# Optimization experiments

Measured on AMD Instinct MI355X. Metric: run time of the kernel, lower is better.

The kernel has to match this reference:

```python
import math
import jax, jax.numpy as jnp
import numpy as np

D_MODEL = 2048
D_INNER = 4096   # expand * d_model
D_STATE = 16
D_CONV = 4
DT_RANK = 128    # d_model / 16
SCALE_X = 0.05         # conv1d input (int8) scale
SCALE_CONV_OUT = 0.05  # conv1d output (int8) scale


def quant(x, scale):
    """Simulated int8 quantize -> dequantize (as in the W4A8 pipeline)."""
    return jnp.clip(jnp.round(x / scale), -128.0, 127.0) * scale


def fwht(x):
    """Normalized fast Walsh-Hadamard transform over the last axis (power of 2)."""
    d = x.shape[-1]
    shp = x.shape
    x = x.reshape(-1, d)
    h = 1
    while h < d:
        x = x.reshape(-1, d // (2 * h), 2, h)
        a, s = x[:, :, 0, :], x[:, :, 1, :]
        x = jnp.stack([a + s, a - s], axis=2).reshape(-1, d)
        h *= 2
    return (x * (d ** -0.5)).reshape(shp)


def setup_inputs() -> dict:
    key = jax.random.key(0)
    ks = jax.random.split(key, 10)
    b, l = 2, 1024
    dt0 = jnp.exp(jax.random.uniform(ks[6], (D_INNER,), minval=math.log(1e-3), maxval=math.log(1e-1)))
    dt_bias = dt0 + jnp.log(-jnp.expm1(-dt0))  # inverse softplus of dt0
    A = -jnp.tile(jnp.arange(1.0, D_STATE + 1.0, dtype=jnp.float32), (D_INNER, 1))
    return {
        "hidden_states": jax.random.normal(ks[0], (b, l, D_MODEL), jnp.float32),
        "W_in": (jax.random.normal(ks[1], (2 * D_INNER, D_MODEL), jnp.float32) * 0.02),
        "conv_w": (jax.random.normal(ks[2], (D_INNER, D_CONV), jnp.float32) * 0.2),
        "conv_b": (jax.random.normal(ks[3], (D_INNER,), jnp.float32) * 0.02),
        "W_x": (jax.random.normal(ks[4], (DT_RANK + 2 * D_STATE, D_INNER), jnp.float32) * 0.02),
        "W_dt": (jax.random.normal(ks[5], (D_INNER, DT_RANK), jnp.float32) * 0.02),
        "dt_bias": dt_bias.astype(jnp.float32),
        "A": A.astype(jnp.float32),
        "D": jnp.ones((D_INNER,), jnp.float32),
        "W_out": (jax.random.normal(ks[7], (D_MODEL, D_INNER), jnp.float32) * 0.02),
    }


def reference(hidden_states, W_in, conv_w, conv_b, W_x, W_dt, dt_bias, A, D, W_out):
    b, l, dm = hidden_states.shape
    # in_proj -> seqlen-last layout, chunk into x (conv path) and z (gate)
    xz = jnp.einsum('bld,ed->bel', hidden_states, W_in)  # [b, 2*d_inner, l]
    x, z = jnp.split(xz, 2, axis=1)                      # [b, d_inner, l] each
    x = quant(x, SCALE_X)                                # int8 activation sim
    # fused causal depthwise conv1d + SiLU + requantize (quant_causal_conv1d)
    xp = jnp.pad(x, ((0, 0), (0, 0), (D_CONV - 1, 0)))
    xc = jax.lax.conv_general_dilated(
        xp, conv_w[:, None, :], (1,), 'VALID',
        dimension_numbers=('NCH', 'OIH', 'NCH'), feature_group_count=D_INNER)
    u = quant(jax.nn.silu(xc + conv_b[None, :, None]), SCALE_CONV_OUT)  # [b,d,l]
    # x_proj -> dt, B, C
    x_dbl = jnp.einsum('bdl,ed->ble', u, W_x)            # [b, l, dt_rank+2n]
    dt_in, B, C = jnp.split(x_dbl, [DT_RANK, DT_RANK + D_STATE], axis=-1)
    dt = jax.nn.softplus(jnp.einsum('blr,dr->bld', dt_in, W_dt) + dt_bias)  # [b,l,d]
    # selective scan: h_t = exp(dt*A) h_{t-1} + dt*B*u ; y = C.h + D*u
    xs = (dt.transpose(1, 0, 2),          # [l,b,d]
          u.transpose(2, 0, 1),           # [l,b,d]
          B.transpose(1, 0, 2),           # [l,b,n]
          C.transpose(1, 0, 2))           # [l,b,n]
    h0 = jnp.zeros((b, D_INNER, D_STATE), hidden_states.dtype)

    def step(h, inp):
        dt_t, u_t, B_t, C_t = inp
        dA = jnp.exp(dt_t[..., None] * A)                       # [b,d,n]
        h = dA * h + (dt_t * u_t)[..., None] * B_t[:, None, :]  # [b,d,n]
        return h, jnp.einsum('bdn,bn->bd', h, C_t)

    _, ys = jax.lax.scan(step, h0, xs)                    # ys: [l,b,d]
    y = ys.transpose(1, 2, 0) + D[:, None] * u            # [b,d,l]
    y = y * jax.nn.silu(z)                                # gated output
    y = fwht(y.transpose(0, 2, 1))                        # Hadamard over channels
    return jnp.einsum('ble,de->bld', y, W_out)            # out_proj -> [b,l,d_model]
```

## Files before the change

### kernel.cpp

```cpp
#include <hip/hip_runtime.h>
#include <math.h>

#define BB 2
#define LL 1024
#define DMODEL 2048
#define DI 4096
#define NSTATE 16
#define RANK 128
#define MM (BB*LL)
#define XE (2*DI)
#define EDBL (RANK + 2*NSTATE)
#define NWORDS (MM*DI/32)
#define NC 16
#define CL (LL/NC)

typedef __bf16 bf16x8 __attribute__((ext_vector_type(8)));
typedef __bf16 bf16x4 __attribute__((ext_vector_type(4)));
typedef float  f32x4  __attribute__((ext_vector_type(4)));

__device__ __forceinline__ float quant005(float x) {
    float q = rintf(x / 0.05f);
    q = fminf(fmaxf(q, -128.f), 127.f);
    return q * 0.05f;
}
__device__ __forceinline__ float softplusf(float x) {
    return fmaxf(x, 0.f) + log1pf(expf(-fabsf(x)));
}

__global__ __launch_bounds__(256) void reduce4g_kernel(
    const float* __restrict__ p, const float* __restrict__ Xx, float* __restrict__ out)
{
    const int gid = blockIdx.x * 256 + threadIdx.x;
    const int m = gid >> 11, c = gid & (DMODEL - 1);
    out[gid] = p[gid] + p[gid + (size_t)MM * DMODEL]
             + Xx[(size_t)m * XE + c] + Xx[(size_t)m * XE + DMODEL + c];
}

__global__ __launch_bounds__(256) void reduce6_kernel(
    const float* __restrict__ p, float* __restrict__ xdbl,
    __bf16* __restrict__ XdH, __bf16* __restrict__ XdM)
{
    const int gid = blockIdx.x * 256 + threadIdx.x;
    const size_t S = (size_t)MM * EDBL;
    float v = p[gid];
    #pragma unroll
    for (int s = 1; s < 6; ++s) v += p[gid + s * S];
    xdbl[gid] = v;
    const int m = gid / EDBL, e = gid - m * EDBL;
    if (e < RANK) {
        const __bf16 h = (__bf16)v;
        XdH[(size_t)m * RANK + e] = h;
        XdM[(size_t)m * RANK + e] = (__bf16)(v - (float)h);
    }
}

__global__ __launch_bounds__(256) void conv_kernel(
    const float* __restrict__ X, const float* __restrict__ conv_w,
    const float* __restrict__ conv_b, float* __restrict__ u,
    __bf16* __restrict__ uh, __bf16* __restrict__ um)
{
    const int gid = blockIdx.x * 256 + threadIdx.x;
    const int bl = gid >> 12, d = gid & (DI - 1);
    const int l = bl & (LL - 1);
    const float4 w4 = *(const float4*)(conv_w + 4 * d);
    const float wk[4] = {w4.x, w4.y, w4.z, w4.w};
    float acc = 0.f;
    #pragma unroll
    for (int k = 0; k < 4; ++k) {
        const int lp = l - 3 + k;
        if (lp >= 0) acc = fmaf(X[(size_t)(bl - 3 + k) * XE + d], wk[k], acc);
    }
    const float v = acc + conv_b[d];
    const float s = v / (1.f + expf(-v));
    const float q = quant005(s);
    u[gid] = q;
    const __bf16 h = (__bf16)q;
    uh[gid] = h;
    um[gid] = (__bf16)(q - (float)h);
}

__global__ __launch_bounds__(256) void scan_p1(
    const float* __restrict__ dtb, const float* __restrict__ u,
    const float* __restrict__ xdbl,
    float* __restrict__ hend, float* __restrict__ S)
{
    const int bx = blockIdx.x;
    const int c  = bx & (NC - 1);
    const int dg = (bx >> 4) & 255;
    const int b  = bx >> 12;
    const int dl = threadIdx.x >> 4, n = threadIdx.x & 15;
    const int d  = (dg << 4) + dl;
    const int t0 = c * CL;
    const float* dtp = dtb + ((size_t)b * LL + t0) * DI + d;
    const float* up  = u   + ((size_t)b * LL + t0) * DI + d;
    const float* xe  = xdbl + ((size_t)b * LL + t0) * EDBL;
    const float An = -(float)(n + 1);
    float h = 0.f, s = 0.f;
    for (int t = 0; t < CL; ++t) {
        const float dt = dtp[(size_t)t * DI];
        const float uv = up[(size_t)t * DI];
        const float Bn = xe[t * EDBL + RANK + n];
        const float w = __expf(dt * An);
        h = fmaf(h, w, dt * uv * Bn);
        s += dt;
    }
    hend[(((size_t)b * DI + d) * NC + c) * 16 + n] = h;
    if (n == 0) S[((size_t)b * DI + d) * NC + c] = s;
}

__global__ __launch_bounds__(256) void scan_p2(
    float* __restrict__ hend, const float* __restrict__ S)
{
    const int gid = blockIdx.x * 256 + threadIdx.x;
    const int n  = gid & 15;
    const int bd = gid >> 4;
    const float An = -(float)(n + 1);
    float* hp = hend + (size_t)bd * NC * 16 + n;
    const float* Sp = S + (size_t)bd * NC;
    float h = 0.f;
    for (int c = 0; c < NC; ++c) {
        const float he = hp[c * 16];
        const float P  = __expf(An * Sp[c]);
        hp[c * 16] = h;
        h = fmaf(h, P, he);
    }
}

__global__ __launch_bounds__(256) void scan_p3(
    const float* __restrict__ dtb, const float* __restrict__ u,
    const float* __restrict__ xdbl, const float* __restrict__ Dvec,
    const float* __restrict__ hin, float* __restrict__ X)
{
    const int bx = blockIdx.x;
    const int c  = bx & (NC - 1);
    const int dg = (bx >> 4) & 255;
    const int b  = bx >> 12;
    const int dl = threadIdx.x >> 4, n = threadIdx.x & 15;
    const int d  = (dg << 4) + dl;
    const int t0 = c * CL;
    const float* dtp = dtb + ((size_t)b * LL + t0) * DI + d;
    const float* up  = u   + ((size_t)b * LL + t0) * DI + d;
    const float* xe  = xdbl + ((size_t)b * LL + t0) * EDBL;
    float* Xp = X + ((size_t)b * LL + t0) * XE + d;
    const float Dv = Dvec[d];
    const float An = -(float)(n + 1);
    float h = hin[(((size_t)b * DI + d) * NC + c) * 16 + n];
    for (int t = 0; t < CL; ++t) {
        const float dt = dtp[(size_t)t * DI];
        const float uv = up[(size_t)t * DI];
        const float* e = xe + t * EDBL;
        const float Bn = e[RANK + n];
        const float Cn = e[RANK + NSTATE + n];
        const float w = __expf(dt * An);
        h = fmaf(h, w, dt * uv * Bn);
        float y = h * Cn;
        y += __shfl_xor(y, 1);
        y += __shfl_xor(y, 2);
        y += __shfl_xor(y, 4);
        y += __shfl_xor(y, 8);
        if (n == 0) {
            const float z = Xp[(size_t)t * XE + DI];
            const float sz = z / (1.f + __expf(-z));
            Xp[(size_t)t * XE] = (y + Dv * uv) * sz;
        }
    }
}

__device__ __forceinline__ void bfy8(float* a)
{
    float t;
    t = a[0]; a[0] = t + a[1]; a[1] = t - a[1];
    t = a[2]; a[2] = t + a[3]; a[3] = t - a[3];
    t = a[4]; a[4] = t + a[5]; a[5] = t - a[5];
    t = a[6]; a[6] = t + a[7]; a[7] = t - a[7];
    t = a[0]; a[0] = t + a[2]; a[2] = t - a[2];
    t = a[1]; a[1] = t + a[3]; a[3] = t - a[3];
    t = a[4]; a[4] = t + a[6]; a[6] = t - a[6];
    t = a[5]; a[5] = t + a[7]; a[7] = t - a[7];
    t = a[0]; a[0] = t + a[4]; a[4] = t - a[4];
    t = a[1]; a[1] = t + a[5]; a[5] = t - a[5];
    t = a[2]; a[2] = t + a[6]; a[6] = t - a[6];
    t = a[3]; a[3] = t + a[7]; a[7] = t - a[7];
}
#define FWIDX(a) ((a) + ((a) >> 5))

__global__ __launch_bounds__(512) void fwht8_kernel(float* __restrict__ X)
{
    __shared__ float s[DI + DI / 32];
    const int tid = threadIdx.x;
    float* base = X + (size_t)blockIdx.x * XE;
    {
        float a[8];
        const float4 v0 = *(const float4*)(base + tid * 8);
        const float4 v1 = *(const float4*)(base + tid * 8 + 4);
        a[0] = v0.x; a[1] = v0.y; a[2] = v0.z; a[3] = v0.w;
        a[4] = v1.x; a[5] = v1.y; a[6] = v1.z; a[7] = v1.w;
        bfy8(a);
        const int p = FWIDX(tid * 8);
        *(float4*)(s + p)     = make_float4(a[0], a[1], a[2], a[3]);
        *(float4*)(s + p + 4) = make_float4(a[4], a[5], a[6], a[7]);
    }
    __syncthreads();
    {
        const int b = (tid >> 3) * 64 + (tid & 7);
        float a[8];
        #pragma unroll
        for (int j = 0; j < 8; ++j) a[j] = s[FWIDX(b + j * 8)];
        bfy8(a);
        #pragma unroll
        for (int j = 0; j < 8; ++j) s[FWIDX(b + j * 8)] = a[j];
    }
    __syncthreads();
    {
        const int b = (tid >> 6) * 512 + (tid & 63);
        float a[8];
        #pragma unroll
        for (int j = 0; j < 8; ++j) a[j] = s[FWIDX(b + j * 64)];
        bfy8(a);
        #pragma unroll
        for (int j = 0; j < 8; ++j) s[FWIDX(b + j * 64)] = a[j];
    }
    __syncthreads();
    {
        const int b = tid;
        float a[8];
        #pragma unroll
        for (int j = 0; j < 8; ++j) a[j] = s[FWIDX(b + j * 512)];
        bfy8(a);
        #pragma unroll
        for (int j = 0; j < 8; ++j) s[FWIDX(b + j * 512)] = a[j];
    }
    __syncthreads();
    const float sc = 1.f / 64.f;
    __bf16* Xh = (__bf16*)(base + DI);
    __bf16* Xm = (__bf16*)(base + DI + 2048);
    for (int i = tid * 2; i < DI; i += 1024) {
        const float v0 = s[FWIDX(i)] * sc, v1 = s[FWIDX(i + 1)] * sc;
        const __bf16 h0 = (__bf16)v0, h1 = (__bf16)v1;
        __bf16 hh[2]  = {h0, h1};
        __bf16 mm2[2] = {(__bf16)(v0 - (float)h0), (__bf16)(v1 - (float)h1)};
        *(short2*)&Xh[i] = *(short2*)hh;
        *(short2*)&Xm[i] = *(short2*)mm2;
    }
}

__global__ __launch_bounds__(256) void splitw_kernel(
    const float* __restrict__ W, __bf16* __restrict__ H, __bf16* __restrict__ L)
{
    const int gid = blockIdx.x * 256 + threadIdx.x;
    const float4 a = *(const float4*)(W + (size_t)gid * 4);
    const float af[4] = {a.x, a.y, a.z, a.w};
    bf16x4 h, l;
    #pragma unroll
    for (int i = 0; i < 4; ++i) {
        const __bf16 hh = (__bf16)af[i];
        h[i] = hh;
        l[i] = (__bf16)(af[i] - (float)hh);
    }
    *(bf16x4*)&H[(size_t)gid * 4] = h;
    *(bf16x4*)&L[(size_t)gid * 4] = l;
}

__global__ __launch_bounds__(256) void splitwx_kernel(
    const float* __restrict__ W, __bf16* __restrict__ H, __bf16* __restrict__ L)
{
    const int gid = blockIdx.x * 256 + threadIdx.x;
    const int row = gid >> 10, c4 = (gid & 1023) << 2;
    float4 a = make_float4(0.f, 0.f, 0.f, 0.f);
    if (row < EDBL) a = *(const float4*)(W + (size_t)row * DI + c4);
    const float af[4] = {a.x, a.y, a.z, a.w};
    bf16x4 h, l;
    #pragma unroll
    for (int i = 0; i < 4; ++i) {
        const __bf16 hh = (__bf16)af[i];
        h[i] = hh;
        l[i] = (__bf16)(af[i] - (float)hh);
    }
    *(bf16x4*)&H[(size_t)(row * DI + c4)] = h;
    *(bf16x4*)&L[(size_t)(row * DI + c4)] = l;
}

__global__ __launch_bounds__(256) void zeromask_kernel(unsigned* __restrict__ mask)
{
    const int gid = blockIdx.x * 256 + threadIdx.x;
    mask[gid] = 0u;
}

__device__ __forceinline__ void stage_tile(const __bf16* __restrict__ g, int ld,
                                           __bf16* lds, int tid)
{
    const int r = tid >> 2;
    const int c = (tid & 3) << 3;
    #pragma unroll
    for (int i = 0; i < 2; ++i) {
        const __bf16* src = g + (size_t)(r + i * 64) * ld + c;
        __builtin_amdgcn_global_load_lds(
            (const __attribute__((address_space(1))) void*)src,
            (__attribute__((address_space(3))) void*)(lds + (r + i * 64) * 32 + c),
            16, 0, 0);
    }
}

template<int EPI>
__global__ __launch_bounds__(256) void gemm3k(
    const __bf16* __restrict__ Ah, const __bf16* __restrict__ Am, int lda,
    const __bf16* __restrict__ Bh, const __bf16* __restrict__ Bm, int ldb,
    float* __restrict__ C, int N, int ldc, int K, int Kz,
    const float* __restrict__ bias)
{
    if (EPI == 2) C += (size_t)blockIdx.z * MM * ldc;
    __shared__ __bf16 sA[128 * 32];
    __shared__ __bf16 sB[128 * 32];
    const int tid  = threadIdx.x;
    const int lane = tid & 63, w = tid >> 6;
    const int wr = w >> 1, wc = w & 1;
    const int bm = blockIdx.y << 7, bn = blockIdx.x << 7;
    const int lr = lane & 15;
    const int kg = (lane >> 4) << 3;
    const int kbeg = blockIdx.z * Kz;

    f32x4 acc[4][4] = {};
    for (int k0 = kbeg; k0 < kbeg + Kz; k0 += 32) {
        const __bf16* Ap; const __bf16* Bp; int kk;
        if (k0 < K)          { Ap = Ah; Bp = Bh; kk = k0; }
        else if (k0 < 2 * K) { Ap = Ah; Bp = Bm; kk = k0 - K; }
        else                 { Ap = Am; Bp = Bh; kk = k0 - 2 * K; }
        stage_tile(Ap + (size_t)bm * lda + kk, lda, sA, tid);
        stage_tile(Bp + (size_t)bn * ldb + kk, ldb, sB, tid);
        __syncthreads();
        bf16x8 a[4], b[4];
        #pragma unroll
        for (int f = 0; f < 4; ++f) {
            a[f] = *(const bf16x8*)&sA[(wr * 64 + f * 16 + lr) * 32 + kg];
            b[f] = *(const bf16x8*)&sB[(wc * 64 + f * 16 + lr) * 32 + kg];
        }
        #pragma unroll
        for (int i = 0; i < 4; ++i)
            #pragma unroll
            for (int j = 0; j < 4; ++j)
                acc[i][j] = __builtin_amdgcn_mfma_f32_16x16x32_bf16(a[i], b[j], acc[i][j], 0, 0, 0);
        __syncthreads();
    }
    #pragma unroll
    for (int i = 0; i < 4; ++i)
        #pragma unroll
        for (int j = 0; j < 4; ++j) {
            const int col  = bn + wc * 64 + j * 16 + (lane & 15);
            const int row0 = bm + wr * 64 + i * 16 + (lane >> 4) * 4;
            #pragma unroll
            for (int r = 0; r < 4; ++r) {
                float v = acc[i][j][r];
                if (EPI == 4) v = softplusf(v + bias[col]);
                if (EPI != 2 || col < N)
                    C[(size_t)(row0 + r) * ldc + col] = v;
            }
        }
}

__device__ __forceinline__ void plane_sel2(int kt, int ktps,
    const __bf16* A0h, const __bf16* A0m, const __bf16* B0h, const __bf16* B0m,
    const __bf16*& Ap, const __bf16*& Bp, int& kc)
{
    if (kt < ktps)          { Ap = A0h; Bp = B0h; kc = kt * 64; }
    else if (kt < 2 * ktps) { Ap = A0h; Bp = B0m; kc = (kt - ktps) * 64; }
    else                    { Ap = A0m; Bp = B0h; kc = (kt - 2 * ktps) * 64; }
}

__device__ __forceinline__ int swz_off(int row, int l16)
{
    const int off = row * 32 + l16 * 8;
    return off ^ (((off >> 6) & 3) << 3);
}

__device__ __forceinline__ void stage_h(
    const __bf16* __restrict__ baseP, const int* goff, int kcol,
    __bf16* ldsHalf, const int* ldso)
{
    #pragma unroll
    for (int i = 0; i < 2; ++i)
        __builtin_amdgcn_global_load_lds(
            (const __attribute__((address_space(1))) void*)(baseP + goff[i] + kcol),
            (__attribute__((address_space(3))) void*)(ldsHalf + ldso[i]),
            16, 0, 0);
}

#define G1BAR  asm volatile("s_barrier" ::: "memory")
#define G1LGKM asm volatile("s_waitcnt lgkmcnt(0)" ::: "memory")
#define G1MFMA(N0, N1)                                                            \
    __builtin_amdgcn_s_setprio(1);                                                \
    _Pragma("unroll")                                                             \
    for (int f = 0; f < 8; ++f) {                                                 \
        acc[f][N0] = __builtin_amdgcn_mfma_f32_16x16x32_bf16(a[f], b0, acc[f][N0], 0, 0, 0); \
        acc[f][N1] = __builtin_amdgcn_mfma_f32_16x16x32_bf16(a[f], b1, acc[f][N1], 0, 0, 0); \
    }                                                                             \
    __builtin_amdgcn_s_setprio(0)

template<int EPI>
__global__ __launch_bounds__(512, 2) void gemm_8p(
    const __bf16* __restrict__ Ah, const __bf16* __restrict__ Am, int lda,
    const __bf16* __restrict__ Bh, const __bf16* __restrict__ Bm, int ldb,
    float* __restrict__ C0, float* __restrict__ C1,
    int ktps, unsigned* __restrict__ mask)
{
    __shared__ __bf16 lds[2][2][2][8192];
    const int tid = threadIdx.x;
    const int lane = tid & 63, w = tid >> 6;
    const int wr = w >> 2, wc = w & 3;
    const int bm = blockIdx.y << 8, bn = blockIdx.x << 8;
    const int lr = lane & 15, l16 = lane >> 4;
    const int T = 3 * ktps;
    const int zoff = (EPI == 2) ? (int)blockIdx.z * 1024 : 0;

    const __bf16* A0h = Ah + (size_t)bm * lda;
    const __bf16* A0m = Am + (size_t)bm * lda;
    const __bf16* B0h = Bh + (size_t)bn * ldb;
    const __bf16* B0m = Bm + (size_t)bn * ldb;

    int ga[2], gb[2], lo[2];
    #pragma unroll
    for (int i = 0; i < 2; ++i) {
        const int t = i * 512 + tid;
        const int row = t >> 2;
        const int gr = (t & 3) ^ ((t >> 3) & 3);
        ga[i] = row * lda + gr * 8;
        gb[i] = row * ldb + gr * 8;
        lo[i] = t * 8;
    }
    int sa[8], sb[4];
    #pragma unroll
    for (int f = 0; f < 8; ++f) sa[f] = swz_off(wr * 128 + f * 16 + lr, l16);
    #pragma unroll
    for (int nf = 0; nf < 4; ++nf) sb[nf] = swz_off(wc * 64 + nf * 16 + lr, l16);

    {
        const __bf16 *Ap, *Bp; int kc;
        plane_sel2(0, ktps, A0h, A0m, B0h, B0m, Ap, Bp, kc);
        stage_h(Ap, ga, zoff + kc +  0, (__bf16*)&lds[0][0][0][0], lo);
        stage_h(Bp, gb, zoff + kc +  0, (__bf16*)&lds[0][1][0][0], lo);
        stage_h(Ap, ga, zoff + kc + 32, (__bf16*)&lds[0][0][1][0], lo);
        stage_h(Bp, gb, zoff + kc + 32, (__bf16*)&lds[0][1][1][0], lo);
        plane_sel2(1, ktps, A0h, A0m, B0h, B0m, Ap, Bp, kc);
        stage_h(Ap, ga, zoff + kc +  0, (__bf16*)&lds[1][0][0][0], lo);
        stage_h(Bp, gb, zoff + kc +  0, (__bf16*)&lds[1][1][0][0], lo);
        stage_h(Ap, ga, zoff + kc + 32, (__bf16*)&lds[1][0][1][0], lo);
    }
    asm volatile("s_waitcnt vmcnt(6)" ::: "memory");
    G1BAR;

    f32x4 acc[8][4] = {};
    for (int kt = 0; kt < T; ++kt) {
        const int c = kt & 1;
        const __bf16* lA = &lds[c][0][0][0];
        const __bf16* lB = &lds[c][1][0][0];
        const __bf16 *Ap2, *Bp2; int kc2;
        plane_sel2(kt + 2 < T ? kt + 2 : T - 1, ktps, A0h, A0m, B0h, B0m, Ap2, Bp2, kc2);
        bf16x8 a[8], b0, b1;

        #pragma unroll
        for (int f = 0; f < 8; ++f) a[f] = *(const bf16x8*)(lA + sa[f]);
        b0 = *(const bf16x8*)(lB + sb[0]);
        b1 = *(const bf16x8*)(lB + sb[1]);
        if (kt + 1 < T) {
            const __bf16 *Ap1, *Bp1; int kc1;
            plane_sel2(kt + 1, ktps, A0h, A0m, B0h, B0m, Ap1, Bp1, kc1);
            stage_h(Bp1, gb, zoff + kc1 + 32, (__bf16*)&lds[c ^ 1][1][1][0], lo);
        }
        G1BAR; G1LGKM;
        G1MFMA(0, 1);
        G1BAR;

        b0 = *(const bf16x8*)(lB + sb[2]);
        b1 = *(const bf16x8*)(lB + sb[3]);
        if (kt + 2 < T)
            stage_h(Ap2, ga, zoff + kc2, (__bf16*)&lds[c][0][0][0], lo);
        G1BAR; G1LGKM;
        G1MFMA(2, 3);
        G1BAR;

        #pragma unroll
        for (int f = 0; f < 8; ++f) a[f] = *(const bf16x8*)(lA + 8192 + sa[f]);
        b0 = *(const bf16x8*)(lB + 8192 + sb[0]);
        b1 = *(const bf16x8*)(lB + 8192 + sb[1]);
        if (kt + 2 < T)
            stage_h(Bp2, gb, zoff + kc2, (__bf16*)&lds[c][1][0][0], lo);
        G1BAR; G1LGKM;
        G1MFMA(0, 1);
        G1BAR;

        b0 = *(const bf16x8*)(lB + 8192 + sb[2]);
        b1 = *(const bf16x8*)(lB + 8192 + sb[3]);
        if (kt + 2 < T)
            stage_h(Ap2, ga, zoff + kc2 + 32, (__bf16*)&lds[c][0][1][0], lo);
        if (kt < T - 2) { asm volatile("s_waitcnt vmcnt(6)" ::: "memory"); }
        else            { asm volatile("s_waitcnt vmcnt(0)" ::: "memory"); }
        G1BAR; G1LGKM;
        G1MFMA(2, 3);
        G1BAR;
    }

    float* Cp; int ldc;
    if (EPI == 1) { Cp = C0; ldc = XE; }
    else {
        if (blockIdx.z < 2) { Cp = C0 + (size_t)blockIdx.z * MM * DMODEL; ldc = DMODEL; }
        else                { Cp = C1 + (size_t)(blockIdx.z - 2) * DMODEL; ldc = XE; }
    }
    #pragma unroll
    for (int f = 0; f < 8; ++f)
        #pragma unroll
        for (int nf = 0; nf < 4; ++nf) {
            const int col  = bn + wc * 64 + nf * 16 + lr;
            const int row0 = bm + wr * 128 + f * 16 + l16 * 4;
            #pragma unroll
            for (int r = 0; r < 4; ++r) {
                float v = acc[f][nf][r];
                const int row = row0 + r;
                if (EPI == 1 && col < DI) {
                    const float fq = v / 0.05f;
                    const float q = rintf(fq);
                    if (0.5f - fabsf(fq - q) < 1e-3f) {
                        const int e = row * DI + col;
                        atomicOr(&mask[e >> 5], 1u << (e & 31));
                    }
                    v = fminf(fmaxf(q, -128.f), 127.f) * 0.05f;
                }
                Cp[(size_t)row * ldc + col] = v;
            }
        }
}

__global__ __launch_bounds__(256) void fixup_kernel(
    const float* __restrict__ hidden, const float* __restrict__ W_in,
    const unsigned* __restrict__ mask, float* __restrict__ X)
{
    const int gwave = (blockIdx.x * 256 + threadIdx.x) >> 6;
    const int lane  = threadIdx.x & 63;
    const int nwaves = gridDim.x * 4;
    for (int base = gwave * 64; base < NWORDS; base += nwaves * 64) {
        const unsigned myw = mask[base + lane];
        unsigned long long bal = __ballot(myw != 0u);
        while (bal) {
            const int src = __ffsll((unsigned long long)bal) - 1;
            bal &= bal - 1;
            unsigned word = __shfl(myw, src);
            const int widx = base + src;
            while (word) {
                const int bit = __ffs(word) - 1;
                word &= word - 1;
                const int e = widx * 32 + bit;
                const int m = e >> 12, n = e & (DI - 1);
                const float* ap = hidden + (size_t)m * DMODEL;
                const float* bp = W_in   + (size_t)n * DMODEL;
                float s = 0.f;
                #pragma unroll
                for (int kk = 0; kk < 8; ++kk) {
                    const int k = kk * 256 + lane * 4;
                    const float4 a = *(const float4*)(ap + k);
                    const float4 b = *(const float4*)(bp + k);
                    s += a.x * b.x + a.y * b.y + a.z * b.z + a.w * b.w;
                }
                s += __shfl_xor(s, 1);  s += __shfl_xor(s, 2);  s += __shfl_xor(s, 4);
                s += __shfl_xor(s, 8);  s += __shfl_xor(s, 16); s += __shfl_xor(s, 32);
                if (lane == 0) X[(size_t)m * XE + n] = quant005(s);
            }
        }
    }
}

extern "C" void kernel_launch(void* const* d_in, const int* in_sizes, int n_in,
                              void* d_out, int out_size, void* d_ws, size_t ws_size,
                              hipStream_t stream)
{
    const float* hidden  = (const float*)d_in[0];
    const float* W_in    = (const float*)d_in[1];
    const float* conv_w  = (const float*)d_in[2];
    const float* conv_b  = (const float*)d_in[3];
    const float* W_x     = (const float*)d_in[4];
    const float* W_dt    = (const float*)d_in[5];
    const float* dt_bias = (const float*)d_in[6];
    const float* Dvec    = (const float*)d_in[8];
    const float* W_out   = (const float*)d_in[9];
    float* out = (float*)d_out;

    float* X    = (float*)d_ws;
    float* u    = X + (size_t)MM * XE;
    float* xdbl = u + (size_t)MM * DI;
    float* dtb  = xdbl + (size_t)MM * EDBL;
    __bf16* WinH  = (__bf16*)u;
    __bf16* WinM  = (__bf16*)dtb;
    unsigned* mask = (unsigned*)xdbl;
    __bf16* uh = (__bf16*)dtb;
    __bf16* um = uh + (size_t)MM * DI;
    __bf16* WoutH = (__bf16*)dtb;
    __bf16* WoutM = WoutH + (size_t)DMODEL * DI;
    float*  part2 = u;
    char* ob = (char*)d_out;
    __bf16* HinH = (__bf16*)ob;
    __bf16* HinM = HinH + (size_t)MM * DMODEL;
    __bf16* WxH  = (__bf16*)ob;
    __bf16* WxM  = WxH + (size_t)256 * DI;
    __bf16* WdtH = (__bf16*)(ob + ((size_t)4 << 20));
    __bf16* WdtM = WdtH + (size_t)DI * RANK;
    __bf16* XdH  = (__bf16*)(ob + ((size_t)6 << 20));
    __bf16* XdM  = XdH + (size_t)MM * RANK;
    float*  xpart = (float*)(ob + ((size_t)7 << 20));
    float* hend = (float*)ob;
    float* Ssum = hend + (size_t)BB * DI * NC * 16;
    const __bf16* Xh = (const __bf16*)(X + DI);
    const __bf16* Xm = (const __bf16*)(X + DI + 2048);

    splitw_kernel<<<2 * DI * DMODEL / 4 / 256, 256, 0, stream>>>(W_in, WinH, WinM);
    splitw_kernel<<<MM * DMODEL / 4 / 256, 256, 0, stream>>>(hidden, HinH, HinM);
    zeromask_kernel<<<NWORDS / 256, 256, 0, stream>>>(mask);
    gemm_8p<1><<<dim3(XE / 256, MM / 256), 512, 0, stream>>>(
        HinH, HinM, DMODEL, WinH, WinM, DMODEL, X, nullptr, 32, mask);
    fixup_kernel<<<256, 256, 0, stream>>>(hidden, W_in, mask, X);
    splitwx_kernel<<<256 * DI / 4 / 256, 256, 0, stream>>>(W_x, WxH, WxM);
    splitw_kernel<<<DI * RANK / 4 / 256, 256, 0, stream>>>(W_dt, WdtH, WdtM);
    conv_kernel<<<MM * DI / 256, 256, 0, stream>>>(X, conv_w, conv_b, u, uh, um);
    gemm3k<2><<<dim3(2, MM / 128, 6), 256, 0, stream>>>(
        uh, um, DI, WxH, WxM, DI, xpart, EDBL, EDBL, DI, 2048, nullptr);
    reduce6_kernel<<<MM * EDBL / 256, 256, 0, stream>>>(xpart, xdbl, XdH, XdM);
    gemm3k<4><<<dim3(DI / 128, MM / 128, 1), 256, 0, stream>>>(
        XdH, XdM, RANK, WdtH, WdtM, RANK, dtb, DI, DI, RANK, 3 * RANK, dt_bias);
    scan_p1<<<BB * 256 * NC, 256, 0, stream>>>(dtb, u, xdbl, hend, Ssum);
    scan_p2<<<BB * DI * 16 / 256, 256, 0, stream>>>(hend, Ssum);
    scan_p3<<<BB * 256 * NC, 256, 0, stream>>>(dtb, u, xdbl, Dvec, hend, X);
    fwht8_kernel<<<MM, 512, 0, stream>>>(X);
    splitw_kernel<<<DMODEL * DI / 4 / 256, 256, 0, stream>>>(W_out, WoutH, WoutM);
    gemm_8p<2><<<dim3(DMODEL / 256, MM / 256, 4), 512, 0, stream>>>(
        Xh, Xm, XE * 2, WoutH, WoutM, DI, part2, X, 16, nullptr);
    reduce4g_kernel<<<MM * DMODEL / 256, 256, 0, stream>>>(part2, X, out);
}
```

Measured before the change: 758.7 us.

## Store conv output as int8, compact FWHT bf16 output, swizzle GEMM block order

Conv now stores the quantized activation as int8 codes instead of fp32, and the scan kernels dequantize on load, cutting scan memory traffic for u by 4x. The FWHT writes its bf16 hi/lo split into separate compact buffers with 8-wide vector stores, so the out-projection GEMM reads contiguous rows with lda=DI instead of strided slices of X. The split-K partials now all go to one contiguous buffer with a simpler 4-way reduce. gemm_8p also remaps workgroup indices with a stride-8 swizzle, likely to spread neighbouring tiles across XCDs or improve cache locality, at some index-math cost.

```diff
diff --git a/kernel.cpp b/kernel.cpp
--- a/kernel.cpp
+++ b/kernel.cpp
@@ -27,13 +27,12 @@
     return fmaxf(x, 0.f) + log1pf(expf(-fabsf(x)));
 }
 
-__global__ __launch_bounds__(256) void reduce4g_kernel(
-    const float* __restrict__ p, const float* __restrict__ Xx, float* __restrict__ out)
+__global__ __launch_bounds__(256) void reduce4_kernel(
+    const float* __restrict__ p, float* __restrict__ out)
 {
     const int gid = blockIdx.x * 256 + threadIdx.x;
-    const int m = gid >> 11, c = gid & (DMODEL - 1);
-    out[gid] = p[gid] + p[gid + (size_t)MM * DMODEL]
-             + Xx[(size_t)m * XE + c] + Xx[(size_t)m * XE + DMODEL + c];
+    const size_t S = (size_t)MM * DMODEL;
+    out[gid] = p[gid] + p[gid + S] + p[gid + 2 * S] + p[gid + 3 * S];
 }
 
 __global__ __launch_bounds__(256) void reduce6_kernel(
@@ -56,7 +55,7 @@
 
 __global__ __launch_bounds__(256) void conv_kernel(
     const float* __restrict__ X, const float* __restrict__ conv_w,
-    const float* __restrict__ conv_b, float* __restrict__ u,
+    const float* __restrict__ conv_b, signed char* __restrict__ u8,
     __bf16* __restrict__ uh, __bf16* __restrict__ um)
 {
     const int gid = blockIdx.x * 256 + threadIdx.x;
@@ -72,15 +71,17 @@
     }
     const float v = acc + conv_b[d];
     const float s = v / (1.f + expf(-v));
-    const float q = quant005(s);
-    u[gid] = q;
+    float qf = rintf(s / 0.05f);
+    qf = fminf(fmaxf(qf, -128.f), 127.f);
+    u8[gid] = (signed char)(int)qf;
+    const float q = qf * 0.05f;
     const __bf16 h = (__bf16)q;
     uh[gid] = h;
     um[gid] = (__bf16)(q - (float)h);
 }
 
 __global__ __launch_bounds__(256) void scan_p1(
-    const float* __restrict__ dtb, const float* __restrict__ u,
+    const float* __restrict__ dtb, const signed char* __restrict__ u8,
     const float* __restrict__ xdbl,
     float* __restrict__ hend, float* __restrict__ S)
 {
@@ -92,13 +93,13 @@
     const int d  = (dg << 4) + dl;
     const int t0 = c * CL;
     const float* dtp = dtb + ((size_t)b * LL + t0) * DI + d;
-    const float* up  = u   + ((size_t)b * LL + t0) * DI + d;
+    const signed char* up = u8 + ((size_t)b * LL + t0) * DI + d;
     const float* xe  = xdbl + ((size_t)b * LL + t0) * EDBL;
     const float An = -(float)(n + 1);
     float h = 0.f, s = 0.f;
     for (int t = 0; t < CL; ++t) {
         const float dt = dtp[(size_t)t * DI];
-        const float uv = up[(size_t)t * DI];
+        const float uv = 0.05f * (float)up[(size_t)t * DI];
         const float Bn = xe[t * EDBL + RANK + n];
         const float w = __expf(dt * An);
         h = fmaf(h, w, dt * uv * Bn);
@@ -127,7 +128,7 @@
 }
 
 __global__ __launch_bounds__(256) void scan_p3(
-    const float* __restrict__ dtb, const float* __restrict__ u,
+    const float* __restrict__ dtb, const signed char* __restrict__ u8,
     const float* __restrict__ xdbl, const float* __restrict__ Dvec,
     const float* __restrict__ hin, float* __restrict__ X)
 {
@@ -139,7 +140,7 @@
     const int d  = (dg << 4) + dl;
     const int t0 = c * CL;
     const float* dtp = dtb + ((size_t)b * LL + t0) * DI + d;
-    const float* up  = u   + ((size_t)b * LL + t0) * DI + d;
+    const signed char* up = u8 + ((size_t)b * LL + t0) * DI + d;
     const float* xe  = xdbl + ((size_t)b * LL + t0) * EDBL;
     float* Xp = X + ((size_t)b * LL + t0) * XE + d;
     const float Dv = Dvec[d];
@@ -147,7 +148,7 @@
     float h = hin[(((size_t)b * DI + d) * NC + c) * 16 + n];
     for (int t = 0; t < CL; ++t) {
         const float dt = dtp[(size_t)t * DI];
-        const float uv = up[(size_t)t * DI];
+        const float uv = 0.05f * (float)up[(size_t)t * DI];
         const float* e = xe + t * EDBL;
         const float Bn = e[RANK + n];
         const float Cn = e[RANK + NSTATE + n];
@@ -184,7 +185,8 @@
 }
 #define FWIDX(a) ((a) + ((a) >> 5))
 
-__global__ __launch_bounds__(512) void fwht8_kernel(float* __restrict__ X)
+__global__ __launch_bounds__(512) void fwht8_kernel(
+    float* __restrict__ X, __bf16* __restrict__ XhC, __bf16* __restrict__ XmC)
 {
     __shared__ float s[DI + DI / 32];
     const int tid = threadIdx.x;
@@ -232,15 +234,21 @@
     }
     __syncthreads();
     const float sc = 1.f / 64.f;
-    __bf16* Xh = (__bf16*)(base + DI);
-    __bf16* Xm = (__bf16*)(base + DI + 2048);
-    for (int i = tid * 2; i < DI; i += 1024) {
-        const float v0 = s[FWIDX(i)] * sc, v1 = s[FWIDX(i + 1)] * sc;
-        const __bf16 h0 = (__bf16)v0, h1 = (__bf16)v1;
-        __bf16 hh[2]  = {h0, h1};
-        __bf16 mm2[2] = {(__bf16)(v0 - (float)h0), (__bf16)(v1 - (float)h1)};
-        *(short2*)&Xh[i] = *(short2*)hh;
-        *(short2*)&Xm[i] = *(short2*)mm2;
+    __bf16* Xh = XhC + (size_t)blockIdx.x * DI;
+    __bf16* Xm = XmC + (size_t)blockIdx.x * DI;
+    {
+        const int i = tid * 8;
+        const float* sp = s + FWIDX(i);
+        bf16x8 hv, mv;
+        #pragma unroll
+        for (int j = 0; j < 8; ++j) {
+            const float v = sp[j] * sc;
+            const __bf16 h = (__bf16)v;
+            hv[j] = h;
+            mv[j] = (__bf16)(v - (float)h);
+        }
+        *(bf16x8*)&Xh[i] = hv;
+        *(bf16x8*)&Xm[i] = mv;
     }
 }
 
@@ -399,17 +407,24 @@
 __global__ __launch_bounds__(512, 2) void gemm_8p(
     const __bf16* __restrict__ Ah, const __bf16* __restrict__ Am, int lda,
     const __bf16* __restrict__ Bh, const __bf16* __restrict__ Bm, int ldb,
-    float* __restrict__ C0, float* __restrict__ C1,
-    int ktps, unsigned* __restrict__ mask)
+    float* __restrict__ C0, int ktps, unsigned* __restrict__ mask)
 {
     __shared__ __bf16 lds[2][2][2][8192];
     const int tid = threadIdx.x;
     const int lane = tid & 63, w = tid >> 6;
     const int wr = w >> 2, wc = w & 3;
-    const int bm = blockIdx.y << 8, bn = blockIdx.x << 8;
     const int lr = lane & 15, l16 = lane >> 4;
     const int T = 3 * ktps;
-    const int zoff = (EPI == 2) ? (int)blockIdx.z * 1024 : 0;
+
+    const int nwg = gridDim.x * gridDim.y * gridDim.z;
+    int flat = ((int)blockIdx.z * gridDim.y + blockIdx.y) * gridDim.x + blockIdx.x;
+    flat = (flat & 7) * (nwg >> 3) + (flat >> 3);
+    const int bxs = flat % gridDim.x;
+    const int tzy = flat / gridDim.x;
+    const int bys = tzy % gridDim.y;
+    const int bzs = tzy / gridDim.y;
+    const int bm = bys << 8, bn = bxs << 8;
+    const int zoff = (EPI == 2) ? bzs * 1024 : 0;
 
     const __bf16* A0h = Ah + (size_t)bm * lda;
     const __bf16* A0m = Am + (size_t)bm * lda;
@@ -500,10 +515,7 @@
 
     float* Cp; int ldc;
     if (EPI == 1) { Cp = C0; ldc = XE; }
-    else {
-        if (blockIdx.z < 2) { Cp = C0 + (size_t)blockIdx.z * MM * DMODEL; ldc = DMODEL; }
-        else                { Cp = C1 + (size_t)(blockIdx.z - 2) * DMODEL; ldc = XE; }
-    }
+    else          { Cp = C0 + (size_t)bzs * MM * DMODEL; ldc = DMODEL; }
     #pragma unroll
     for (int f = 0; f < 8; ++f)
         #pragma unroll
@@ -588,11 +600,14 @@
     __bf16* WinH  = (__bf16*)u;
     __bf16* WinM  = (__bf16*)dtb;
     unsigned* mask = (unsigned*)xdbl;
+    signed char* u8 = (signed char*)u;
     __bf16* uh = (__bf16*)dtb;
     __bf16* um = uh + (size_t)MM * DI;
     __bf16* WoutH = (__bf16*)dtb;
     __bf16* WoutM = WoutH + (size_t)DMODEL * DI;
-    float*  part2 = u;
+    __bf16* XhC = (__bf16*)u;
+    __bf16* XmC = XhC + (size_t)MM * DI;
+    float*  part4 = X;
     char* ob = (char*)d_out;
     __bf16* HinH = (__bf16*)ob;
     __bf16* HinM = HinH + (size_t)MM * DMODEL;
@@ -605,29 +620,27 @@
     float*  xpart = (float*)(ob + ((size_t)7 << 20));
     float* hend = (float*)ob;
     float* Ssum = hend + (size_t)BB * DI * NC * 16;
-    const __bf16* Xh = (const __bf16*)(X + DI);
-    const __bf16* Xm = (const __bf16*)(X + DI + 2048);
 
     splitw_kernel<<<2 * DI * DMODEL / 4 / 256, 256, 0, stream>>>(W_in, WinH, WinM);
     splitw_kernel<<<MM * DMODEL / 4 / 256, 256, 0, stream>>>(hidden, HinH, HinM);
     zeromask_kernel<<<NWORDS / 256, 256, 0, stream>>>(mask);
     gemm_8p<1><<<dim3(XE / 256, MM / 256), 512, 0, stream>>>(
-        HinH, HinM, DMODEL, WinH, WinM, DMODEL, X, nullptr, 32, mask);
+        HinH, HinM, DMODEL, WinH, WinM, DMODEL, X, 32, mask);
     fixup_kernel<<<256, 256, 0, stream>>>(hidden, W_in, mask, X);
     splitwx_kernel<<<256 * DI / 4 / 256, 256, 0, stream>>>(W_x, WxH, WxM);
     splitw_kernel<<<DI * RANK / 4 / 256, 256, 0, stream>>>(W_dt, WdtH, WdtM);
-    conv_kernel<<<MM * DI / 256, 256, 0, stream>>>(X, conv_w, conv_b, u, uh, um);
+    conv_kernel<<<MM * DI / 256, 256, 0, stream>>>(X, conv_w, conv_b, u8, uh, um);
     gemm3k<2><<<dim3(2, MM / 128, 6), 256, 0, stream>>>(
         uh, um, DI, WxH, WxM, DI, xpart, EDBL, EDBL, DI, 2048, nullptr);
     reduce6_kernel<<<MM * EDBL / 256, 256, 0, stream>>>(xpart, xdbl, XdH, XdM);
     gemm3k<4><<<dim3(DI / 128, MM / 128, 1), 256, 0, stream>>>(
         XdH, XdM, RANK, WdtH, WdtM, RANK, dtb, DI, DI, RANK, 3 * RANK, dt_bias);
-    scan_p1<<<BB * 256 * NC, 256, 0, stream>>>(dtb, u, xdbl, hend, Ssum);
+    scan_p1<<<BB * 256 * NC, 256, 0, stream>>>(dtb, u8, xdbl, hend, Ssum);
     scan_p2<<<BB * DI * 16 / 256, 256, 0, stream>>>(hend, Ssum);
-    scan_p3<<<BB * 256 * NC, 256, 0, stream>>>(dtb, u, xdbl, Dvec, hend, X);
-    fwht8_kernel<<<MM, 512, 0, stream>>>(X);
+    scan_p3<<<BB * 256 * NC, 256, 0, stream>>>(dtb, u8, xdbl, Dvec, hend, X);
+    fwht8_kernel<<<MM, 512, 0, stream>>>(X, XhC, XmC);
     splitw_kernel<<<DMODEL * DI / 4 / 256, 256, 0, stream>>>(W_out, WoutH, WoutM);
     gemm_8p<2><<<dim3(DMODEL / 256, MM / 256, 4), 512, 0, stream>>>(
-        Xh, Xm, XE * 2, WoutH, WoutM, DI, part2, X, 16, nullptr);
-    reduce4g_kernel<<<MM * DMODEL / 256, 256, 0, stream>>>(part2, X, out);
-}
+        XhC, XmC, DI, WoutH, WoutM, DI, part4, 16, nullptr);
+    reduce4_kernel<<<MM * DMODEL / 256, 256, 0, stream>>>(part4, out);
+}
```

Measured after the change: 759.3 us. About the same (+0.1%).
